# Optimization experiments

Measured on AMD Instinct MI355X. Metric: run time of the kernel, lower is better.

## Reference

```python
import jax, jax.numpy as jnp
import numpy as np

NUM_EXPERT = 16
IN_FEAT = 2048
OUT_FEAT = 8192
TOTAL_TOKENS = 8192


def _make_counts(rng, num_expert, total):
    # random partition of `total` tokens into `num_expert` contiguous groups
    cuts = np.sort(rng.integers(0, total + 1, size=num_expert - 1))
    counts = np.diff(np.concatenate([[0], cuts, [total]]))
    return counts.astype(np.int64)


def setup_inputs() -> dict:
    key = jax.random.key(0)
    k_inp, k_w = jax.random.split(key)
    inp = jax.random.normal(k_inp, (TOTAL_TOKENS, IN_FEAT), dtype=jnp.float32)
    # kaiming-uniform style init matching reset_parameters (fan_in = IN_FEAT)
    bound = np.sqrt(3.0) * (np.sqrt(2.0 / (1.0 + 5.0)) / np.sqrt(IN_FEAT))
    weight = jax.random.uniform(
        k_w, (NUM_EXPERT, OUT_FEAT, IN_FEAT), dtype=jnp.float32,
        minval=-bound, maxval=bound)
    rng = np.random.default_rng(0)
    fwd_expert_count = jnp.asarray(_make_counts(rng, NUM_EXPERT, TOTAL_TOKENS))
    return {"inp": inp, "weight": weight, "fwd_expert_count": fwd_expert_count}


def reference(inp, weight, fwd_expert_count):
    # Grouped GEMM: tokens are laid out contiguously per expert; group e of
    # size fwd_expert_count[e] is multiplied by weight[e]^T ([out,in] -> x@W^T).
    # fwd_expert_count is routing metadata (host-side int constants in FastMoE),
    # so slice bounds are static Python ints.
    counts = np.asarray(fwd_expert_count)
    offsets = np.concatenate([[0], np.cumsum(counts)])
    outs = []
    for e in range(weight.shape[0]):  # small fixed expert loop
        n = int(counts[e])
        seg = jax.lax.dynamic_slice_in_dim(inp, int(offsets[e]), n, axis=0)
        outs.append(jnp.einsum('ti,oi->to', seg, weight[e]))
    return jnp.concatenate(outs, axis=0)  # [total_tokens, out_feat]
```

## Files before the change

### kernel.cpp

```cpp
#include <hip/hip_runtime.h>
#include <stdint.h>
#include <stddef.h>

#define NUM_EXPERT 16
#define IN_FEAT 2048
#define OUT_FEAT 8192
#define TOTAL_TOKENS 8192

#define BM 256
#define BN 128
#define BK 32
#define KSTEPS (IN_FEAT / BK)
#define NT_TILES (OUT_FEAT / BN)
#define MAX_SLOTS 48

typedef __attribute__((ext_vector_type(8))) short short8;
typedef __attribute__((ext_vector_type(4))) float floatx4;
typedef __attribute__((ext_vector_type(4))) uint32_t uintx4;

__device__ __forceinline__ uint32_t pk_bf16(float a, float b) {
    uint32_t ua = __float_as_uint(a) + 0x8000u;
    uint32_t ub = __float_as_uint(b) + 0x8000u;
    return __builtin_amdgcn_perm(ub, ua, 0x07060302u);
}

__device__ __forceinline__ void cp16_to_lds(const void* g, void* l) {
    __builtin_amdgcn_global_load_lds(
        (const __attribute__((address_space(1))) uint32_t*)g,
        (__attribute__((address_space(3))) uint32_t*)l, 16, 0, 0);
}

__global__ __launch_bounds__(256) void cvt_a_kernel(const float* __restrict__ inp,
                                                    uint16_t* __restrict__ dst) {
    size_t base = ((size_t)blockIdx.x * 256 + threadIdx.x) * 8;
    floatx4 f0 = ((const floatx4*)(inp + base))[0];
    floatx4 f1 = ((const floatx4*)(inp + base))[1];
    uintx4 d;
    d.x = pk_bf16(f0.x, f0.y);
    d.y = pk_bf16(f0.z, f0.w);
    d.z = pk_bf16(f1.x, f1.y);
    d.w = pk_bf16(f1.z, f1.w);
    *(uintx4*)(dst + base) = d;
}

template <bool A_IN_WS>
__global__ __launch_bounds__(512, 4)
void moe_gemm(const float* __restrict__ W,
              const float* __restrict__ inp,
              const uint16_t* __restrict__ Abf,
              const int* __restrict__ cnt_raw,
              float* __restrict__ out) {
    const int nwg = (int)gridDim.x;
    const int orig = (int)blockIdx.x;
    const int wgid = (orig & 7) * (nwg >> 3) + (orig >> 3);
    const int slot = wgid % MAX_SLOTS;
    const int nt = wgid / MAX_SLOTS;

    int sum32 = 0;
#pragma unroll
    for (int i = 0; i < NUM_EXPERT; ++i) sum32 += cnt_raw[i];
    const int idxmul = (sum32 == TOTAL_TOKENS) ? 1 : 2;

    int e = -1, lt = 0, cnt = 0, row0 = 0;
    {
        int off = 0, tacc = 0;
#pragma unroll
        for (int i = 0; i < NUM_EXPERT; ++i) {
            int c = cnt_raw[i * idxmul];
            int t = (c + BM - 1) >> 8;
            if (e < 0 && slot < tacc + t) {
                e = i; lt = slot - tacc; cnt = c; row0 = off + lt * BM;
            }
            tacc += t; off += c;
        }
    }
    if (e < 0) return;

    const int tid = (int)threadIdx.x;
    const int lane = tid & 63;
    const int w = tid >> 6;
    const int wm = w & 3;
    const int wn = w >> 2;
    const int l15 = lane & 15;
    const int l4 = lane >> 4;

    __shared__ uint16_t Abuf[2][BM * BK];
    __shared__ uint16_t Bbuf[2][BN * BK];

    const int bn_ = tid & (BN - 1);
    const int bp_ = tid >> 7;
    const float* bg = W + ((size_t)e * OUT_FEAT + (size_t)nt * BN + bn_) * IN_FEAT + bp_ * 8;
    const int boff = (bp_ * BN + bn_) * 8;

    const uint16_t* ag0 = nullptr; const uint16_t* ag1 = nullptr;
    int aoff0 = 0, aoff1 = 0;
    const float* ia = nullptr;
    int foff0 = 0, foff1 = 0;
    if constexpr (A_IN_WS) {
        int c0 = tid, c1 = 512 + tid;
        int r0 = c0 & 255, p0 = c0 >> 8;
        int r1 = c1 & 255, p1 = c1 >> 8;
        int gr0 = min(row0 + r0, TOTAL_TOKENS - 1);
        int gr1 = min(row0 + r1, TOTAL_TOKENS - 1);
        ag0 = Abf + (size_t)gr0 * IN_FEAT + p0 * 8;
        ag1 = Abf + (size_t)gr1 * IN_FEAT + p1 * 8;
        aoff0 = (w * 64) * 8;
        aoff1 = (512 + w * 64) * 8;
    } else {
        int r = tid & 255;
        int pb = (tid >> 8) * 2;
        int gr = min(row0 + r, TOTAL_TOKENS - 1);
        ia = inp + (size_t)gr * IN_FEAT + pb * 8;
        foff0 = (pb * 256 + r) * 8;
        foff1 = ((pb + 1) * 256 + r) * 8;
    }

    int aidx[4], bidx[4];
#pragma unroll
    for (int i = 0; i < 4; ++i) aidx[i] = l4 * 256 + wm * 64 + i * 16 + l15;
#pragma unroll
    for (int j = 0; j < 4; ++j) bidx[j] = l4 * 128 + wn * 64 + j * 16 + l15;

    floatx4 acc[4][4] = {};

    {
        floatx4 b0 = ((const floatx4*)bg)[0];
        floatx4 b1 = ((const floatx4*)bg)[1];
        if constexpr (A_IN_WS) {
            cp16_to_lds(ag0, Abuf[0] + aoff0);
            cp16_to_lds(ag1, Abuf[0] + aoff1);
            ag0 += BK; ag1 += BK;
        } else {
            floatx4 a0 = ((const floatx4*)ia)[0];
            floatx4 a1 = ((const floatx4*)ia)[1];
            floatx4 a2 = ((const floatx4*)ia)[2];
            floatx4 a3 = ((const floatx4*)ia)[3];
            uintx4 da0, da1;
            da0.x = pk_bf16(a0.x, a0.y); da0.y = pk_bf16(a0.z, a0.w);
            da0.z = pk_bf16(a1.x, a1.y); da0.w = pk_bf16(a1.z, a1.w);
            da1.x = pk_bf16(a2.x, a2.y); da1.y = pk_bf16(a2.z, a2.w);
            da1.z = pk_bf16(a3.x, a3.y); da1.w = pk_bf16(a3.z, a3.w);
            *(uintx4*)(Abuf[0] + foff0) = da0;
            *(uintx4*)(Abuf[0] + foff1) = da1;
            ia += BK;
        }
        uintx4 db;
        db.x = pk_bf16(b0.x, b0.y); db.y = pk_bf16(b0.z, b0.w);
        db.z = pk_bf16(b1.x, b1.y); db.w = pk_bf16(b1.z, b1.w);
        *(uintx4*)(Bbuf[0] + boff) = db;
        bg += BK;
        __syncthreads();
    }

    for (int ks = 0; ks < KSTEPS - 1; ++ks) {
        const int cur = ks & 1, nxt = cur ^ 1;

        floatx4 b0 = ((const floatx4*)bg)[0];
        floatx4 b1 = ((const floatx4*)bg)[1];
        floatx4 a0, a1, a2, a3;
        if constexpr (A_IN_WS) {
            cp16_to_lds(ag0, Abuf[nxt] + aoff0);
            cp16_to_lds(ag1, Abuf[nxt] + aoff1);
            ag0 += BK; ag1 += BK;
        } else {
            a0 = ((const floatx4*)ia)[0];
            a1 = ((const floatx4*)ia)[1];
            a2 = ((const floatx4*)ia)[2];
            a3 = ((const floatx4*)ia)[3];
            ia += BK;
        }
        bg += BK;

        const short8* Ach = (const short8*)Abuf[cur];
        const short8* Bch = (const short8*)Bbuf[cur];
        short8 av[4], bv[4];
#pragma unroll
        for (int j = 0; j < 4; ++j) bv[j] = Bch[bidx[j]];
#pragma unroll
        for (int i = 0; i < 4; ++i) av[i] = Ach[aidx[i]];
#pragma unroll
        for (int i = 0; i < 4; ++i)
#pragma unroll
            for (int j = 0; j < 4; ++j)
                acc[i][j] = __builtin_amdgcn_mfma_f32_16x16x32_bf16(av[i], bv[j], acc[i][j], 0, 0, 0);

        if constexpr (!A_IN_WS) {
            uintx4 da0, da1;
            da0.x = pk_bf16(a0.x, a0.y); da0.y = pk_bf16(a0.z, a0.w);
            da0.z = pk_bf16(a1.x, a1.y); da0.w = pk_bf16(a1.z, a1.w);
            da1.x = pk_bf16(a2.x, a2.y); da1.y = pk_bf16(a2.z, a2.w);
            da1.z = pk_bf16(a3.x, a3.y); da1.w = pk_bf16(a3.z, a3.w);
            *(uintx4*)(Abuf[nxt] + foff0) = da0;
            *(uintx4*)(Abuf[nxt] + foff1) = da1;
        }
        {
            uintx4 db;
            db.x = pk_bf16(b0.x, b0.y); db.y = pk_bf16(b0.z, b0.w);
            db.z = pk_bf16(b1.x, b1.y); db.w = pk_bf16(b1.z, b1.w);
            *(uintx4*)(Bbuf[nxt] + boff) = db;
        }
        __syncthreads();
    }

    {
        const short8* Ach = (const short8*)Abuf[1];
        const short8* Bch = (const short8*)Bbuf[1];
        short8 av[4], bv[4];
#pragma unroll
        for (int j = 0; j < 4; ++j) bv[j] = Bch[bidx[j]];
#pragma unroll
        for (int i = 0; i < 4; ++i) av[i] = Ach[aidx[i]];
#pragma unroll
        for (int i = 0; i < 4; ++i)
#pragma unroll
            for (int j = 0; j < 4; ++j)
                acc[i][j] = __builtin_amdgcn_mfma_f32_16x16x32_bf16(av[i], bv[j], acc[i][j], 0, 0, 0);
    }

    const int cnt_loc = cnt - lt * BM;
    const size_t col = (size_t)nt * BN + wn * 64 + l15;
#pragma unroll
    for (int i = 0; i < 4; ++i) {
        int rb = wm * 64 + i * 16 + l4 * 4;
#pragma unroll
        for (int reg = 0; reg < 4; ++reg) {
            int r = rb + reg;
            if (r < cnt_loc) {
                float* rp = out + (size_t)(row0 + r) * OUT_FEAT + col;
                rp[0]  = acc[i][0][reg];
                rp[16] = acc[i][1][reg];
                rp[32] = acc[i][2][reg];
                rp[48] = acc[i][3][reg];
            }
        }
    }
}

extern "C" void kernel_launch(void* const* d_in, const int* in_sizes, int n_in,
                              void* d_out, int out_size, void* d_ws, size_t ws_size,
                              hipStream_t stream) {
    const float* inp = (const float*)d_in[0];
    const float* W = (const float*)d_in[1];
    const int* counts = (const int*)d_in[2];
    float* out = (float*)d_out;

    const size_t abytes = (size_t)TOTAL_TOKENS * IN_FEAT * sizeof(uint16_t);
    dim3 grid(NT_TILES * MAX_SLOTS);

    if (ws_size >= abytes) {
        uint16_t* Abf = (uint16_t*)d_ws;
        int nblk = (int)(((size_t)TOTAL_TOKENS * IN_FEAT) / (256 * 8));
        cvt_a_kernel<<<nblk, 256, 0, stream>>>(inp, Abf);
        moe_gemm<true><<<grid, 512, 0, stream>>>(W, inp, Abf, counts, out);
    } else {
        moe_gemm<false><<<grid, 512, 0, stream>>>(W, inp, nullptr, counts, out);
    }
}
```

Baseline: 2.161 ms.

## Add triple-buffered async LDS pipeline with 256x256 tiles for grouped GEMM

Replaces the workspace-path GEMM with a kernel that streams both the bf16 A tile and raw fp32 weights straight into LDS through global_load_lds. It uses three buffers with a vmcnt wait, so loads for step t+2 overlap compute on step t. The weights are converted to bf16 while being read from LDS instead of in registers before the store. The N tile doubles to 256 so each workgroup does more MFMA per byte loaded, and s_setprio brackets the MFMA bursts. In exchange the kernel uses a lot of LDS (48KB A plus 96KB fp32 B), runs fewer blocks per CU, and converts B redundantly across waves.

```diff
diff --git a/kernel.cpp b/kernel.cpp
--- a/kernel.cpp
+++ b/kernel.cpp
@@ -8,15 +8,17 @@
 #define TOTAL_TOKENS 8192
 
 #define BM 256
-#define BN 128
+#define BN 256
 #define BK 32
-#define KSTEPS (IN_FEAT / BK)
+#define NKT (IN_FEAT / BK)
 #define NT_TILES (OUT_FEAT / BN)
 #define MAX_SLOTS 48
 
 typedef __attribute__((ext_vector_type(8))) short short8;
 typedef __attribute__((ext_vector_type(4))) float floatx4;
 typedef __attribute__((ext_vector_type(4))) uint32_t uintx4;
+
+union UCast { uintx4 u; short8 s; };
 
 __device__ __forceinline__ uint32_t pk_bf16(float a, float b) {
     uint32_t ua = __float_as_uint(a) + 0x8000u;
@@ -43,13 +45,11 @@
     *(uintx4*)(dst + base) = d;
 }
 
-template <bool A_IN_WS>
-__global__ __launch_bounds__(512, 4)
-void moe_gemm(const float* __restrict__ W,
-              const float* __restrict__ inp,
-              const uint16_t* __restrict__ Abf,
-              const int* __restrict__ cnt_raw,
-              float* __restrict__ out) {
+__global__ __launch_bounds__(512, 2)
+void moe_gemm_pipe(const float* __restrict__ W,
+                   const uint16_t* __restrict__ Abf,
+                   const int* __restrict__ cnt_raw,
+                   float* __restrict__ out) {
     const int nwg = (int)gridDim.x;
     const int orig = (int)blockIdx.x;
     const int wgid = (orig & 7) * (nwg >> 3) + (orig >> 3);
@@ -79,41 +79,170 @@
     const int tid = (int)threadIdx.x;
     const int lane = tid & 63;
     const int w = tid >> 6;
+    const int wm = w & 1;
+    const int wn = w >> 1;
+    const int l15 = lane & 15;
+    const int l4 = lane >> 4;
+
+    __shared__ uint16_t Ash[3 * 8192];
+    __shared__ float    Bsh[3 * 8192];
+
+    const int ar = tid & 255;
+    const int ap = tid >> 8;
+    const int gr = min(row0 + ar, TOTAL_TOKENS - 1);
+    const uint16_t* aS = Abf + (size_t)gr * IN_FEAT + ap * 8;
+    const float* bS = W + ((size_t)e * OUT_FEAT + (size_t)nt * BN + ar) * IN_FEAT + ap * 4;
+    const int aDc = w * 64;
+    const int bDc = w * 64;
+
+    int aidx[8];
+#pragma unroll
+    for (int mi = 0; mi < 8; ++mi) aidx[mi] = l4 * 256 + wm * 128 + mi * 16 + l15;
+    int bidx[4];
+#pragma unroll
+    for (int nj = 0; nj < 4; ++nj) bidx[nj] = l4 * 512 + wn * 64 + nj * 16 + l15;
+
+    floatx4 acc[8][4] = {};
+
+#pragma unroll
+    for (int t0 = 0; t0 < 2; ++t0) {
+        const uint16_t* ap_ = aS + t0 * BK;
+        uint16_t* ad = &Ash[0] + t0 * 8192 + aDc * 8;
+        cp16_to_lds(ap_,      ad);
+        cp16_to_lds(ap_ + 16, ad + 512 * 8);
+        const float* bp_ = bS + t0 * BK;
+        float* bd = &Bsh[0] + t0 * 8192 + bDc * 4;
+        cp16_to_lds(bp_,      bd);
+        cp16_to_lds(bp_ + 8,  bd + 512 * 4);
+        cp16_to_lds(bp_ + 16, bd + 1024 * 4);
+        cp16_to_lds(bp_ + 24, bd + 1536 * 4);
+    }
+
+    int cb = 0;
+    for (int t = 0; t < NKT; ++t) {
+        const int sb = (cb + 2 >= 3) ? cb - 1 : cb + 2;
+
+        asm volatile("s_waitcnt vmcnt(6)" ::: "memory");
+        __builtin_amdgcn_s_barrier();
+        asm volatile("" ::: "memory");
+
+        {
+            const int kts = (t + 2 < NKT) ? t + 2 : NKT - 1;
+            const uint16_t* ap_ = aS + kts * BK;
+            uint16_t* ad = &Ash[0] + sb * 8192 + aDc * 8;
+            cp16_to_lds(ap_,      ad);
+            cp16_to_lds(ap_ + 16, ad + 512 * 8);
+            const float* bp_ = bS + kts * BK;
+            float* bd = &Bsh[0] + sb * 8192 + bDc * 4;
+            cp16_to_lds(bp_,      bd);
+            cp16_to_lds(bp_ + 8,  bd + 512 * 4);
+            cp16_to_lds(bp_ + 16, bd + 1024 * 4);
+            cp16_to_lds(bp_ + 24, bd + 1536 * 4);
+        }
+
+        const short8* Ach = (const short8*)(&Ash[0] + cb * 8192);
+        const floatx4* Bf = (const floatx4*)(&Bsh[0] + cb * 8192);
+
+        short8 bv[4];
+#pragma unroll
+        for (int nj = 0; nj < 4; ++nj) {
+            floatx4 lo = Bf[bidx[nj]];
+            floatx4 hi = Bf[bidx[nj] + 256];
+            UCast u;
+            u.u.x = pk_bf16(lo.x, lo.y); u.u.y = pk_bf16(lo.z, lo.w);
+            u.u.z = pk_bf16(hi.x, hi.y); u.u.w = pk_bf16(hi.z, hi.w);
+            bv[nj] = u.s;
+        }
+#pragma unroll
+        for (int g = 0; g < 2; ++g) {
+            short8 av[4];
+#pragma unroll
+            for (int k = 0; k < 4; ++k) av[k] = Ach[aidx[g * 4 + k]];
+            __builtin_amdgcn_s_setprio(1);
+#pragma unroll
+            for (int k = 0; k < 4; ++k)
+#pragma unroll
+                for (int nj = 0; nj < 4; ++nj)
+                    acc[g * 4 + k][nj] = __builtin_amdgcn_mfma_f32_16x16x32_bf16(
+                        av[k], bv[nj], acc[g * 4 + k][nj], 0, 0, 0);
+            __builtin_amdgcn_s_setprio(0);
+        }
+
+        cb = (cb + 1 >= 3) ? 0 : cb + 1;
+    }
+
+    const int cnt_loc = cnt - lt * BM;
+    const size_t col = (size_t)nt * BN + wn * 64 + l15;
+#pragma unroll
+    for (int mi = 0; mi < 8; ++mi) {
+        int rb = wm * 128 + mi * 16 + l4 * 4;
+#pragma unroll
+        for (int reg = 0; reg < 4; ++reg) {
+            int r = rb + reg;
+            if (r < cnt_loc) {
+                float* rp = out + (size_t)(row0 + r) * OUT_FEAT + col;
+                rp[0]  = acc[mi][0][reg];
+                rp[16] = acc[mi][1][reg];
+                rp[32] = acc[mi][2][reg];
+                rp[48] = acc[mi][3][reg];
+            }
+        }
+    }
+}
+
+__global__ __launch_bounds__(512, 4)
+void moe_gemm_fb(const float* __restrict__ W,
+                 const float* __restrict__ inp,
+                 const int* __restrict__ cnt_raw,
+                 float* __restrict__ out) {
+    const int nwg = (int)gridDim.x;
+    const int orig = (int)blockIdx.x;
+    const int wgid = (orig & 7) * (nwg >> 3) + (orig >> 3);
+    const int slot = wgid % 48;
+    const int nt = wgid / 48;
+
+    int sum32 = 0;
+#pragma unroll
+    for (int i = 0; i < NUM_EXPERT; ++i) sum32 += cnt_raw[i];
+    const int idxmul = (sum32 == TOTAL_TOKENS) ? 1 : 2;
+
+    int e = -1, lt = 0, cnt = 0, row0 = 0;
+    {
+        int off = 0, tacc = 0;
+#pragma unroll
+        for (int i = 0; i < NUM_EXPERT; ++i) {
+            int c = cnt_raw[i * idxmul];
+            int t = (c + 255) >> 8;
+            if (e < 0 && slot < tacc + t) {
+                e = i; lt = slot - tacc; cnt = c; row0 = off + lt * 256;
+            }
+            tacc += t; off += c;
+        }
+    }
+    if (e < 0) return;
+
+    const int tid = (int)threadIdx.x;
+    const int lane = tid & 63;
+    const int w = tid >> 6;
     const int wm = w & 3;
     const int wn = w >> 2;
     const int l15 = lane & 15;
     const int l4 = lane >> 4;
 
-    __shared__ uint16_t Abuf[2][BM * BK];
-    __shared__ uint16_t Bbuf[2][BN * BK];
-
-    const int bn_ = tid & (BN - 1);
+    __shared__ uint16_t Abuf[2][256 * 32];
+    __shared__ uint16_t Bbuf[2][128 * 32];
+
+    const int bn_ = tid & 127;
     const int bp_ = tid >> 7;
-    const float* bg = W + ((size_t)e * OUT_FEAT + (size_t)nt * BN + bn_) * IN_FEAT + bp_ * 8;
-    const int boff = (bp_ * BN + bn_) * 8;
-
-    const uint16_t* ag0 = nullptr; const uint16_t* ag1 = nullptr;
-    int aoff0 = 0, aoff1 = 0;
-    const float* ia = nullptr;
-    int foff0 = 0, foff1 = 0;
-    if constexpr (A_IN_WS) {
-        int c0 = tid, c1 = 512 + tid;
-        int r0 = c0 & 255, p0 = c0 >> 8;
-        int r1 = c1 & 255, p1 = c1 >> 8;
-        int gr0 = min(row0 + r0, TOTAL_TOKENS - 1);
-        int gr1 = min(row0 + r1, TOTAL_TOKENS - 1);
-        ag0 = Abf + (size_t)gr0 * IN_FEAT + p0 * 8;
-        ag1 = Abf + (size_t)gr1 * IN_FEAT + p1 * 8;
-        aoff0 = (w * 64) * 8;
-        aoff1 = (512 + w * 64) * 8;
-    } else {
-        int r = tid & 255;
-        int pb = (tid >> 8) * 2;
-        int gr = min(row0 + r, TOTAL_TOKENS - 1);
-        ia = inp + (size_t)gr * IN_FEAT + pb * 8;
-        foff0 = (pb * 256 + r) * 8;
-        foff1 = ((pb + 1) * 256 + r) * 8;
-    }
+    const float* bg = W + ((size_t)e * OUT_FEAT + (size_t)nt * 128 + bn_) * IN_FEAT + bp_ * 8;
+    const int boff = (bp_ * 128 + bn_) * 8;
+
+    int r = tid & 255;
+    int pb = (tid >> 8) * 2;
+    int grr = min(row0 + r, TOTAL_TOKENS - 1);
+    const float* ia = inp + (size_t)grr * IN_FEAT + pb * 8;
+    const int foff0 = (pb * 256 + r) * 8;
+    const int foff1 = ((pb + 1) * 256 + r) * 8;
 
     int aidx[4], bidx[4];
 #pragma unroll
@@ -126,50 +255,35 @@
     {
         floatx4 b0 = ((const floatx4*)bg)[0];
         floatx4 b1 = ((const floatx4*)bg)[1];
-        if constexpr (A_IN_WS) {
-            cp16_to_lds(ag0, Abuf[0] + aoff0);
-            cp16_to_lds(ag1, Abuf[0] + aoff1);
-            ag0 += BK; ag1 += BK;
-        } else {
-            floatx4 a0 = ((const floatx4*)ia)[0];
-            floatx4 a1 = ((const floatx4*)ia)[1];
-            floatx4 a2 = ((const floatx4*)ia)[2];
-            floatx4 a3 = ((const floatx4*)ia)[3];
-            uintx4 da0, da1;
-            da0.x = pk_bf16(a0.x, a0.y); da0.y = pk_bf16(a0.z, a0.w);
-            da0.z = pk_bf16(a1.x, a1.y); da0.w = pk_bf16(a1.z, a1.w);
-            da1.x = pk_bf16(a2.x, a2.y); da1.y = pk_bf16(a2.z, a2.w);
-            da1.z = pk_bf16(a3.x, a3.y); da1.w = pk_bf16(a3.z, a3.w);
-            *(uintx4*)(Abuf[0] + foff0) = da0;
-            *(uintx4*)(Abuf[0] + foff1) = da1;
-            ia += BK;
-        }
+        floatx4 a0 = ((const floatx4*)ia)[0];
+        floatx4 a1 = ((const floatx4*)ia)[1];
+        floatx4 a2 = ((const floatx4*)ia)[2];
+        floatx4 a3 = ((const floatx4*)ia)[3];
+        uintx4 da0, da1;
+        da0.x = pk_bf16(a0.x, a0.y); da0.y = pk_bf16(a0.z, a0.w);
+        da0.z = pk_bf16(a1.x, a1.y); da0.w = pk_bf16(a1.z, a1.w);
+        da1.x = pk_bf16(a2.x, a2.y); da1.y = pk_bf16(a2.z, a2.w);
+        da1.z = pk_bf16(a3.x, a3.y); da1.w = pk_bf16(a3.z, a3.w);
+        *(uintx4*)(Abuf[0] + foff0) = da0;
+        *(uintx4*)(Abuf[0] + foff1) = da1;
+        ia += 32;
         uintx4 db;
         db.x = pk_bf16(b0.x, b0.y); db.y = pk_bf16(b0.z, b0.w);
         db.z = pk_bf16(b1.x, b1.y); db.w = pk_bf16(b1.z, b1.w);
         *(uintx4*)(Bbuf[0] + boff) = db;
-        bg += BK;
+        bg += 32;
         __syncthreads();
     }
 
-    for (int ks = 0; ks < KSTEPS - 1; ++ks) {
+    for (int ks = 0; ks < 63; ++ks) {
         const int cur = ks & 1, nxt = cur ^ 1;
-
         floatx4 b0 = ((const floatx4*)bg)[0];
         floatx4 b1 = ((const floatx4*)bg)[1];
-        floatx4 a0, a1, a2, a3;
-        if constexpr (A_IN_WS) {
-            cp16_to_lds(ag0, Abuf[nxt] + aoff0);
-            cp16_to_lds(ag1, Abuf[nxt] + aoff1);
-            ag0 += BK; ag1 += BK;
-        } else {
-            a0 = ((const floatx4*)ia)[0];
-            a1 = ((const floatx4*)ia)[1];
-            a2 = ((const floatx4*)ia)[2];
-            a3 = ((const floatx4*)ia)[3];
-            ia += BK;
-        }
-        bg += BK;
+        floatx4 a0 = ((const floatx4*)ia)[0];
+        floatx4 a1 = ((const floatx4*)ia)[1];
+        floatx4 a2 = ((const floatx4*)ia)[2];
+        floatx4 a3 = ((const floatx4*)ia)[3];
+        ia += 32; bg += 32;
 
         const short8* Ach = (const short8*)Abuf[cur];
         const short8* Bch = (const short8*)Bbuf[cur];
@@ -184,21 +298,17 @@
             for (int j = 0; j < 4; ++j)
                 acc[i][j] = __builtin_amdgcn_mfma_f32_16x16x32_bf16(av[i], bv[j], acc[i][j], 0, 0, 0);
 
-        if constexpr (!A_IN_WS) {
-            uintx4 da0, da1;
-            da0.x = pk_bf16(a0.x, a0.y); da0.y = pk_bf16(a0.z, a0.w);
-            da0.z = pk_bf16(a1.x, a1.y); da0.w = pk_bf16(a1.z, a1.w);
-            da1.x = pk_bf16(a2.x, a2.y); da1.y = pk_bf16(a2.z, a2.w);
-            da1.z = pk_bf16(a3.x, a3.y); da1.w = pk_bf16(a3.z, a3.w);
-            *(uintx4*)(Abuf[nxt] + foff0) = da0;
-            *(uintx4*)(Abuf[nxt] + foff1) = da1;
-        }
-        {
-            uintx4 db;
-            db.x = pk_bf16(b0.x, b0.y); db.y = pk_bf16(b0.z, b0.w);
-            db.z = pk_bf16(b1.x, b1.y); db.w = pk_bf16(b1.z, b1.w);
-            *(uintx4*)(Bbuf[nxt] + boff) = db;
-        }
+        uintx4 da0, da1;
+        da0.x = pk_bf16(a0.x, a0.y); da0.y = pk_bf16(a0.z, a0.w);
+        da0.z = pk_bf16(a1.x, a1.y); da0.w = pk_bf16(a1.z, a1.w);
+        da1.x = pk_bf16(a2.x, a2.y); da1.y = pk_bf16(a2.z, a2.w);
+        da1.z = pk_bf16(a3.x, a3.y); da1.w = pk_bf16(a3.z, a3.w);
+        *(uintx4*)(Abuf[nxt] + foff0) = da0;
+        *(uintx4*)(Abuf[nxt] + foff1) = da1;
+        uintx4 db;
+        db.x = pk_bf16(b0.x, b0.y); db.y = pk_bf16(b0.z, b0.w);
+        db.z = pk_bf16(b1.x, b1.y); db.w = pk_bf16(b1.z, b1.w);
+        *(uintx4*)(Bbuf[nxt] + boff) = db;
         __syncthreads();
     }
 
@@ -217,16 +327,16 @@
                 acc[i][j] = __builtin_amdgcn_mfma_f32_16x16x32_bf16(av[i], bv[j], acc[i][j], 0, 0, 0);
     }
 
-    const int cnt_loc = cnt - lt * BM;
-    const size_t col = (size_t)nt * BN + wn * 64 + l15;
+    const int cnt_loc = cnt - lt * 256;
+    const size_t col = (size_t)nt * 128 + wn * 64 + l15;
 #pragma unroll
     for (int i = 0; i < 4; ++i) {
         int rb = wm * 64 + i * 16 + l4 * 4;
 #pragma unroll
         for (int reg = 0; reg < 4; ++reg) {
-            int r = rb + reg;
-            if (r < cnt_loc) {
-                float* rp = out + (size_t)(row0 + r) * OUT_FEAT + col;
+            int rr = rb + reg;
+            if (rr < cnt_loc) {
+                float* rp = out + (size_t)(row0 + rr) * OUT_FEAT + col;
                 rp[0]  = acc[i][0][reg];
                 rp[16] = acc[i][1][reg];
                 rp[32] = acc[i][2][reg];
@@ -245,14 +355,15 @@
     float* out = (float*)d_out;
 
     const size_t abytes = (size_t)TOTAL_TOKENS * IN_FEAT * sizeof(uint16_t);
-    dim3 grid(NT_TILES * MAX_SLOTS);
 
     if (ws_size >= abytes) {
         uint16_t* Abf = (uint16_t*)d_ws;
         int nblk = (int)(((size_t)TOTAL_TOKENS * IN_FEAT) / (256 * 8));
         cvt_a_kernel<<<nblk, 256, 0, stream>>>(inp, Abf);
-        moe_gemm<true><<<grid, 512, 0, stream>>>(W, inp, Abf, counts, out);
+        dim3 grid(NT_TILES * MAX_SLOTS);
+        moe_gemm_pipe<<<grid, 512, 0, stream>>>(W, Abf, counts, out);
     } else {
-        moe_gemm<false><<<grid, 512, 0, stream>>>(W, inp, nullptr, counts, out);
-    }
-}
+        dim3 grid(64 * 48);
+        moe_gemm_fb<<<grid, 512, 0, stream>>>(W, inp, counts, out);
+    }
+}
```

Result: slower. 2.217 ms (+2.6%).
